# Optimization experiments

Measured on AMD Instinct MI355X. Metric: run time of the kernel, lower is better.

The kernel has to match this reference:

```python
import jax, jax.numpy as jnp
import numpy as np

B, LQ, LKV, D, H = 4, 1024, 2048, 1024, 16
HD = D // H
EPS = 1e-5
NEG = -1e9


def _layernorm(x, w, b):
    mu = jnp.mean(x, axis=-1, keepdims=True)
    var = jnp.mean(jnp.square(x - mu), axis=-1, keepdims=True)
    return (x - mu) * jax.lax.rsqrt(var + EPS) * w + b


def setup_inputs() -> dict:
    key = jax.random.key(0)
    ks = jax.random.split(key, 10)
    q = jax.random.normal(ks[0], (B, LQ, D), dtype=jnp.float32)
    kv = jax.random.normal(ks[1], (B, LKV, D), dtype=jnp.float32)
    # ragged kv lengths; mask True == padding
    lengths = jax.random.randint(ks[2], (B,), LKV // 4, LKV + 1)
    mask = jnp.arange(LKV)[None, :] >= lengths[:, None]  # [B, LKV] bool
    s = 1.0 / np.sqrt(D)
    params = dict(
        norm_q_w=jnp.ones((D,), jnp.float32),
        norm_q_b=jnp.zeros((D,), jnp.float32),
        norm_kv_w=jnp.ones((D,), jnp.float32),
        norm_kv_b=jnp.zeros((D,), jnp.float32),
        Wq=jax.random.normal(ks[3], (D, D), jnp.float32) * s,
        bq=jnp.zeros((D,), jnp.float32),
        Wkv=jax.random.normal(ks[4], (2 * D, D), jnp.float32) * s,
        bkv=jnp.zeros((2 * D,), jnp.float32),
        Wo=jax.random.normal(ks[5], (D, D), jnp.float32) * s,
        bo=jnp.zeros((D,), jnp.float32),
    )
    return dict(q=q, kv=kv, mask=mask, **params)


def reference(q, kv, mask, norm_q_w, norm_q_b, norm_kv_w, norm_kv_b, Wq, bq, Wkv, bkv, Wo, bo):
    q_res = q
    qn = _layernorm(q, norm_q_w, norm_q_b)
    kvn = _layernorm(kv, norm_kv_w, norm_kv_b)
    # projections
    qh = (qn @ Wq.T + bq).reshape(B, LQ, H, HD)
    kvp = (kvn @ Wkv.T + bkv).reshape(B, LKV, 2, H, HD)
    k, v = kvp[:, :, 0], kvp[:, :, 1]  # [B, LKV, H, HD]
    # masked cross attention (math-equivalent to varlen flash attn over unpadded kv)
    scale = 1.0 / np.sqrt(HD)
    scores = jnp.einsum('bqhd,bkhd->bhqk', qh, k) * scale
    scores = jnp.where(mask[:, None, None, :], NEG, scores)
    attn = jax.nn.softmax(scores, axis=-1)
    out = jnp.einsum('bhqk,bkhd->bqhd', attn, v).reshape(B, LQ, D)
    # out proj + residual (dropout is identity in eval)
    return q_res + (out @ Wo.T + bo)


if __name__ == '__main__':
    inp = setup_inputs()
    y = reference(**inp)
    print(y.shape, y.dtype)
```

## Files before the change

kernel.cpp:

```cpp
#include <hip/hip_runtime.h>

#define DEV __device__ __forceinline__

typedef unsigned short u16;
typedef float  floatx4 __attribute__((ext_vector_type(4)));
typedef unsigned int uintx2 __attribute__((ext_vector_type(2)));
typedef unsigned int uintx4 __attribute__((ext_vector_type(4)));
typedef __bf16 bf16x8 __attribute__((ext_vector_type(8)));

constexpr int cB = 4, cLQ = 1024, cLKV = 2048, cD = 1024, cH = 16, cHD = 64;

DEV u16 f2bf(float f) {
  unsigned u = __builtin_bit_cast(unsigned, f);
  u += 0x7fffu + ((u >> 16) & 1u);
  return (u16)(u >> 16);
}

DEV bf16x8 ld_frag(const u16* p) {
  uintx4 u = *(const uintx4*)p;
  return __builtin_bit_cast(bf16x8, u);
}

DEV floatx4 mfma16(bf16x8 a, bf16x8 b, floatx4 c) {
  return __builtin_amdgcn_mfma_f32_16x16x32_bf16(a, b, c, 0, 0, 0);
}

DEV float ex2(float x) { return __builtin_amdgcn_exp2f(x); }

DEV unsigned pkbf(float a, float b) {
  return (__builtin_bit_cast(unsigned, b) & 0xffff0000u) |
         (__builtin_bit_cast(unsigned, a) >> 16);
}

DEV void pl32(unsigned &a, unsigned &b) {
#if __has_builtin(__builtin_amdgcn_permlane32_swap)
  uintx2 r = __builtin_amdgcn_permlane32_swap(a, b, false, false);
  a = r[0]; b = r[1];
#else
  asm("v_permlane32_swap_b32 %0, %1" : "+v"(a), "+v"(b));
#endif
}
DEV void pl16(unsigned &a, unsigned &b) {
#if __has_builtin(__builtin_amdgcn_permlane16_swap)
  uintx2 r = __builtin_amdgcn_permlane16_swap(a, b, false, false);
  a = r[0]; b = r[1];
#else
  asm("v_permlane16_swap_b32 %0, %1" : "+v"(a), "+v"(b));
#endif
}

__global__ __launch_bounds__(256) void prep_kernel(
    const float* __restrict__ q, const float* __restrict__ kv,
    const float* __restrict__ nqw, const float* __restrict__ nqb,
    const float* __restrict__ nkw, const float* __restrict__ nkb,
    u16* __restrict__ qn, u16* __restrict__ kvn,
    const float* __restrict__ Wq, const float* __restrict__ Wkv,
    const float* __restrict__ Wo, u16* __restrict__ wqb,
    u16* __restrict__ wkvb, u16* __restrict__ wob,
    const void* __restrict__ mask, int* __restrict__ lens) {
  int bid = blockIdx.x, tid = threadIdx.x;
  if (bid < 3072) {
    int row = bid * 4 + (tid >> 6);
    int lane = tid & 63;
    const float* x; const float* w; const float* b; u16* dst;
    if (row < cB * cLQ) {
      x = q + (size_t)row * cD; w = nqw; b = nqb; dst = qn + (size_t)row * cD;
    } else {
      int r2 = row - cB * cLQ;
      x = kv + (size_t)r2 * cD; w = nkw; b = nkb; dst = kvn + (size_t)r2 * cD;
    }
    const float4* xf = (const float4*)x;
    float4 v[4];
    #pragma unroll
    for (int c = 0; c < 4; c++) v[c] = xf[lane + 64 * c];
    float s = 0.f;
    #pragma unroll
    for (int c = 0; c < 4; c++) s += (v[c].x + v[c].y) + (v[c].z + v[c].w);
    #pragma unroll
    for (int m = 1; m < 64; m <<= 1) s += __shfl_xor(s, m, 64);
    float mean = s * (1.f / cD);
    float ss = 0.f;
    #pragma unroll
    for (int c = 0; c < 4; c++) {
      v[c].x -= mean; v[c].y -= mean; v[c].z -= mean; v[c].w -= mean;
      ss += (v[c].x * v[c].x + v[c].y * v[c].y) +
            (v[c].z * v[c].z + v[c].w * v[c].w);
    }
    #pragma unroll
    for (int m = 1; m < 64; m <<= 1) ss += __shfl_xor(ss, m, 64);
    float rs = rsqrtf(ss * (1.f / cD) + 1e-5f);
    const float4* wf = (const float4*)w;
    const float4* bf = (const float4*)b;
    #pragma unroll
    for (int c = 0; c < 4; c++) {
      float4 wv = wf[lane + 64 * c];
      float4 bv = bf[lane + 64 * c];
      ushort4 o;
      o.x = f2bf(v[c].x * rs * wv.x + bv.x);
      o.y = f2bf(v[c].y * rs * wv.y + bv.y);
      o.z = f2bf(v[c].z * rs * wv.z + bv.z);
      o.w = f2bf(v[c].w * rs * wv.w + bv.w);
      ((ushort4*)dst)[lane + 64 * c] = o;
    }
  } else if (bid < 4096) {
    int base = (bid - 3072) * 1024;
    #pragma unroll
    for (int c = 0; c < 4; c++) {
      int gi = base + c * 256 + tid;
      const float* src; u16* dst; int off;
      if (gi < 262144)      { src = Wq;  dst = wqb;  off = gi; }
      else if (gi < 786432) { src = Wkv; dst = wkvb; off = gi - 262144; }
      else                  { src = Wo;  dst = wob;  off = gi - 786432; }
      float4 v = ((const float4*)src)[off];
      ushort4 o;
      o.x = f2bf(v.x); o.y = f2bf(v.y); o.z = f2bf(v.z); o.w = f2bf(v.w);
      ((ushort4*)dst)[off] = o;
    }
  } else {
    __shared__ int smode;
    __shared__ int cnt[cB];
    if (tid == 0) smode = 0;
    if (tid < cB) cnt[tid] = 0;
    __syncthreads();
    const unsigned* mi = (const unsigned*)mask;
    int bad = 0;
    for (int i = tid; i < cB * cLKV / 4; i += 256)
      if (mi[i] > 1u) bad = 1;
    if (bad) smode = 1;
    __syncthreads();
    if (smode == 0) {
      for (int b = 0; b < cB; b++) {
        int c = 0;
        for (int i = tid; i < cLKV; i += 256) c += (mi[(size_t)b * cLKV + i] == 0u);
        atomicAdd(&cnt[b], c);
      }
    } else {
      const unsigned char* m8 = (const unsigned char*)mask;
      for (int b = 0; b < cB; b++) {
        int c = 0;
        for (int i = tid; i < cLKV; i += 256) c += (m8[(size_t)b * cLKV + i] == 0);
        atomicAdd(&cnt[b], c);
      }
    }
    __syncthreads();
    if (tid < cB) lens[tid] = cnt[tid];
    if (tid == 0) {
      int ord[4] = {0, 1, 2, 3};
      #pragma unroll
      for (int a = 0; a < 3; a++)
        #pragma unroll
        for (int d = 0; d < 3; d++)
          if (cnt[ord[d]] < cnt[ord[d + 1]]) {
            int tswap = ord[d]; ord[d] = ord[d + 1]; ord[d + 1] = tswap;
          }
      #pragma unroll
      for (int a = 0; a < 4; a++) lens[4 + a] = ord[a];
    }
  }
}

struct TileCtx {
  int m16, quad, wr, wc;
};

DEV void gemm_mainloop(const u16* __restrict__ A, const u16* __restrict__ Bm,
                       int row0, int col0, int K, u16* As, u16* Bs,
                       const TileCtx& t, floatx4 (&acc)[4][4]) {
  int tid = threadIdx.x;
  int wave = tid >> 6, lane = tid & 63;
  int srow = wave * 16 + (lane >> 2);
  int sseg = (lane & 3) * 8;
  const u16* ga = A + (size_t)(row0 + srow) * K + sseg;
  const u16* gb = Bm + (size_t)(col0 + srow) * K + sseg;
  const size_t rstep = (size_t)64 * K;
  int woff = srow * 32 + sseg;

  uintx4 a0 = *(const uintx4*)ga;
  uintx4 a1 = *(const uintx4*)(ga + rstep);
  uintx4 b0 = *(const uintx4*)gb;
  uintx4 b1 = *(const uintx4*)(gb + rstep);
  *(uintx4*)(As + woff) = a0;
  *(uintx4*)(As + woff + 2048) = a1;
  *(uintx4*)(Bs + woff) = b0;
  *(uintx4*)(Bs + woff + 2048) = b1;
  a0 = *(const uintx4*)(ga + 32);
  a1 = *(const uintx4*)(ga + rstep + 32);
  b0 = *(const uintx4*)(gb + 32);
  b1 = *(const uintx4*)(gb + rstep + 32);
  __syncthreads();

  for (int k0 = 0; k0 < K; k0 += 32) {
    int cur = (k0 >> 5) & 1;
    const u16* rA = As + cur * 4096;
    const u16* rB = Bs + cur * 4096;
    bf16x8 af[4], bfr[4];
    #pragma unroll
    for (int i = 0; i < 4; i++)
      af[i] = ld_frag(&rA[(t.wr * 64 + i * 16 + t.m16) * 32 + t.quad * 8]);
    #pragma unroll
    for (int j = 0; j < 4; j++)
      bfr[j] = ld_frag(&rB[(t.wc * 64 + j * 16 + t.m16) * 32 + t.quad * 8]);
    if (k0 + 32 < K) {
      u16* nA = As + (cur ^ 1) * 4096 + woff;
      u16* nB = Bs + (cur ^ 1) * 4096 + woff;
      *(uintx4*)nA = a0;
      *(uintx4*)(nA + 2048) = a1;
      *(uintx4*)nB = b0;
      *(uintx4*)(nB + 2048) = b1;
      if (k0 + 64 < K) {
        a0 = *(const uintx4*)(ga + k0 + 64);
        a1 = *(const uintx4*)(ga + rstep + k0 + 64);
        b0 = *(const uintx4*)(gb + k0 + 64);
        b1 = *(const uintx4*)(gb + rstep + k0 + 64);
      }
    }
    #pragma unroll
    for (int i = 0; i < 4; i++)
      #pragma unroll
      for (int j = 0; j < 4; j++)
        acc[i][j] = mfma16(af[i], bfr[j], acc[i][j]);
    __syncthreads();
  }
}

__global__ __launch_bounds__(256) void proj_fused(
    const u16* __restrict__ qn, const u16* __restrict__ wqb,
    const float* __restrict__ bq, u16* __restrict__ qhb,
    const u16* __restrict__ kvn, const u16* __restrict__ wkvb,
    const float* __restrict__ bkv, u16* __restrict__ khb,
    u16* __restrict__ vthb, const int* __restrict__ lens) {
  __shared__ __align__(16) u16 As[2 * 128 * 32];
  __shared__ __align__(16) u16 Bs[2 * 128 * 32];
  int bid = blockIdx.x;
  int lane = threadIdx.x & 63;
  TileCtx t;
  t.m16 = lane & 15; t.quad = lane >> 4;
  int wave = threadIdx.x >> 6;
  t.wr = wave >> 1; t.wc = wave & 1;

  bool isQ = bid < 256;
  int row0, col0;
  const u16* A; const u16* Bm; const float* bias;
  if (isQ) {
    row0 = (bid >> 3) * 128; col0 = (bid & 7) * 128;
    A = qn; Bm = wqb; bias = bq;
  } else {
    int b2 = bid - 256;
    row0 = (b2 >> 4) * 128; col0 = (b2 & 15) * 128;
    A = kvn; Bm = wkvb; bias = bkv;
    if ((row0 & (cLKV - 1)) >= lens[row0 >> 11]) return;
  }

  floatx4 z = {0.f, 0.f, 0.f, 0.f};
  floatx4 acc[4][4];
  #pragma unroll
  for (int i = 0; i < 4; i++)
    #pragma unroll
    for (int j = 0; j < 4; j++) acc[i][j] = z;

  gemm_mainloop(A, Bm, row0, col0, cD, As, Bs, t, acc);

  #pragma unroll
  for (int j = 0; j < 4; j++) {
    int col = col0 + t.wc * 64 + j * 16 + t.m16;
    float bs = bias[col];
    if (isQ) {
      #pragma unroll
      for (int i = 0; i < 4; i++) {
        int crow = row0 + t.wr * 64 + i * 16 + t.quad * 4;
        #pragma unroll
        for (int r = 0; r < 4; r++)
          qhb[(size_t)(crow + r) * cD + col] =
              f2bf((acc[i][j][r] + bs) * 0.18033688f);
      }
    } else {
      bool isK = col < cD;
      int c2 = isK ? col : col - cD;
      int hh = c2 >> 6, dd = c2 & 63;
      #pragma unroll
      for (int i = 0; i < 4; i++) {
        int crow = row0 + t.wr * 64 + i * 16 + t.quad * 4;
        int bb = crow >> 11, kvp = crow & (cLKV - 1);
        if (isK) {
          u16* dst = khb + ((size_t)(bb * cH + hh) * cLKV + kvp) * 64 + dd;
          #pragma unroll
          for (int r = 0; r < 4; r++) dst[(size_t)r * 64] = f2bf(acc[i][j][r] + bs);
        } else {
          u16* dst = vthb + ((size_t)(bb * cH + hh) * 64 + dd) * cLKV + kvp;
          ushort4 o;
          o.x = f2bf(acc[i][j][0] + bs);
          o.y = f2bf(acc[i][j][1] + bs);
          o.z = f2bf(acc[i][j][2] + bs);
          o.w = f2bf(acc[i][j][3] + bs);
          *(ushort4*)dst = o;
        }
      }
    }
  }
}

__global__ __launch_bounds__(256) void gemm_o(
    const u16* __restrict__ A, const u16* __restrict__ Bm,
    const float* __restrict__ bias, const float* __restrict__ res,
    float* __restrict__ Cout, int N, int K) {
  __shared__ __align__(16) u16 As[2 * 64 * 32];
  __shared__ __align__(16) u16 Bs[2 * 128 * 32];
  int lane = threadIdx.x & 63;
  int m16 = lane & 15, quad = lane >> 4;
  int wave = threadIdx.x >> 6;
  int wr = wave >> 1, wc = wave & 1;
  int row0 = blockIdx.y * 64, col0 = blockIdx.x * 128;

  int tid = threadIdx.x;
  int srow = tid >> 2;
  int sseg = (tid & 3) * 8;
  const u16* ga = A + (size_t)(row0 + srow) * K + sseg;
  const u16* gb = Bm + (size_t)(col0 + srow) * K + sseg;
  const size_t rstep = (size_t)64 * K;
  int woff = srow * 32 + sseg;

  uintx4 a0 = *(const uintx4*)ga;
  uintx4 b0 = *(const uintx4*)gb;
  uintx4 b1 = *(const uintx4*)(gb + rstep);
  *(uintx4*)(As + woff) = a0;
  *(uintx4*)(Bs + woff) = b0;
  *(uintx4*)(Bs + woff + 2048) = b1;
  a0 = *(const uintx4*)(ga + 32);
  b0 = *(const uintx4*)(gb + 32);
  b1 = *(const uintx4*)(gb + rstep + 32);
  __syncthreads();

  floatx4 z = {0.f, 0.f, 0.f, 0.f};
  floatx4 acc[2][4];
  #pragma unroll
  for (int i = 0; i < 2; i++)
    #pragma unroll
    for (int j = 0; j < 4; j++) acc[i][j] = z;

  for (int k0 = 0; k0 < K; k0 += 32) {
    int cur = (k0 >> 5) & 1;
    const u16* rA = As + cur * 2048;
    const u16* rB = Bs + cur * 4096;
    bf16x8 af[2], bfr[4];
    #pragma unroll
    for (int i = 0; i < 2; i++)
      af[i] = ld_frag(&rA[(wr * 32 + i * 16 + m16) * 32 + quad * 8]);
    #pragma unroll
    for (int j = 0; j < 4; j++)
      bfr[j] = ld_frag(&rB[(wc * 64 + j * 16 + m16) * 32 + quad * 8]);
    if (k0 + 32 < K) {
      u16* nA = As + (cur ^ 1) * 2048 + woff;
      u16* nB = Bs + (cur ^ 1) * 4096 + woff;
      *(uintx4*)nA = a0;
      *(uintx4*)nB = b0;
      *(uintx4*)(nB + 2048) = b1;
      if (k0 + 64 < K) {
        a0 = *(const uintx4*)(ga + k0 + 64);
        b0 = *(const uintx4*)(gb + k0 + 64);
        b1 = *(const uintx4*)(gb + rstep + k0 + 64);
      }
    }
    #pragma unroll
    for (int i = 0; i < 2; i++)
      #pragma unroll
      for (int j = 0; j < 4; j++)
        acc[i][j] = mfma16(af[i], bfr[j], acc[i][j]);
    __syncthreads();
  }

  #pragma unroll
  for (int j = 0; j < 4; j++) {
    int col = col0 + wc * 64 + j * 16 + m16;
    float bs = bias[col];
    #pragma unroll
    for (int i = 0; i < 2; i++) {
      int crow = row0 + wr * 32 + i * 16 + quad * 4;
      #pragma unroll
      for (int r = 0; r < 4; r++) {
        size_t idx = (size_t)(crow + r) * N + col;
        Cout[idx] = acc[i][j][r] + bs + res[idx];
      }
    }
  }
}

constexpr int KS = 72;

template<bool MASK>
DEV void attn_compute(int k0, int len, const u16* __restrict__ Kt,
                      const u16* __restrict__ Vt,
                      const bf16x8 (&qf)[2][2], int m16, int quad,
                      float (&lsum)[2], floatx4 (&accO)[2][4]) {
  floatx4 z = {0.f, 0.f, 0.f, 0.f};
  bf16x8 kf[4][2];
  #pragma unroll
  for (int t = 0; t < 4; t++) {
    kf[t][0] = ld_frag(&Kt[(t * 16 + m16) * KS + quad * 8]);
    kf[t][1] = ld_frag(&Kt[(t * 16 + m16) * KS + 32 + quad * 8]);
  }
  floatx4 s[2][4];
  #pragma unroll
  for (int g = 0; g < 2; g++)
    #pragma unroll
    for (int t = 0; t < 4; t++) {
      floatx4 tt = z;
      tt = mfma16(kf[t][0], qf[g][0], tt);
      tt = mfma16(kf[t][1], qf[g][1], tt);
      s[g][t] = tt;
    }
  bf16x8 ap0[2], ap1[2];
  #pragma unroll
  for (int g = 0; g < 2; g++) {
    unsigned p[4][2];
    #pragma unroll
    for (int t = 0; t < 4; t++) {
      float e0, e1, e2, e3;
      if (MASK) {
        int key = k0 + t * 16 + quad * 4;
        e0 = (key     < len) ? ex2(s[g][t][0]) : 0.f;
        e1 = (key + 1 < len) ? ex2(s[g][t][1]) : 0.f;
        e2 = (key + 2 < len) ? ex2(s[g][t][2]) : 0.f;
        e3 = (key + 3 < len) ? ex2(s[g][t][3]) : 0.f;
      } else {
        e0 = ex2(s[g][t][0]);
        e1 = ex2(s[g][t][1]);
        e2 = ex2(s[g][t][2]);
        e3 = ex2(s[g][t][3]);
      }
      lsum[g] += (e0 + e1) + (e2 + e3);
      p[t][0] = pkbf(e0, e1);
      p[t][1] = pkbf(e2, e3);
    }
    unsigned a0 = p[0][0], b0 = p[1][0]; pl32(a0, b0); pl16(a0, b0);
    unsigned a1 = p[0][1], b1 = p[1][1]; pl32(a1, b1); pl16(a1, b1);
    uintx4 lo = {a0, a1, b0, b1};
    unsigned c0 = p[2][0], d0 = p[3][0]; pl32(c0, d0); pl16(c0, d0);
    unsigned c1 = p[2][1], d1 = p[3][1]; pl32(c1, d1); pl16(c1, d1);
    uintx4 hi = {c0, c1, d0, d1};
    ap0[g] = __builtin_bit_cast(bf16x8, lo);
    ap1[g] = __builtin_bit_cast(bf16x8, hi);
  }
  #pragma unroll
  for (int db = 0; db < 4; db++) {
    bf16x8 bv0 = ld_frag(&Vt[(db * 16 + m16) * KS + quad * 8]);
    bf16x8 bv1 = ld_frag(&Vt[(db * 16 + m16) * KS + 32 + quad * 8]);
    #pragma unroll
    for (int g = 0; g < 2; g++) {
      accO[g][db] = mfma16(ap0[g], bv0, accO[g][db]);
      accO[g][db] = mfma16(ap1[g], bv1, accO[g][db]);
    }
  }
}

__global__ __launch_bounds__(256) void attn_kernel(
    const u16* __restrict__ qh, const u16* __restrict__ kh,
    const u16* __restrict__ vth, const int* __restrict__ lens,
    u16* __restrict__ out) {
  int bid = blockIdx.x;
  int r = bid >> 7;
  int rank = r ^ (r >> 1);
  int b = lens[4 + rank];
  int combo = bid & 127;
  int h = combo >> 3;
  int qt = combo & 7;
  int len = lens[b];
  int wave = threadIdx.x >> 6, lane = threadIdx.x & 63;
  int m16 = lane & 15, quad = lane >> 4;

  __shared__ __align__(16) u16 Kt[64 * KS];
  __shared__ __align__(16) u16 Vt[64 * KS];

  int q0 = qt * 128 + wave * 32;
  const u16* qp = qh + ((size_t)(b * cLQ + q0 + m16) * cH + h) * cHD;
  bf16x8 qf[2][2];
  qf[0][0] = ld_frag(qp + quad * 8);
  qf[0][1] = ld_frag(qp + 32 + quad * 8);
  qf[1][0] = ld_frag(qp + (size_t)16 * cD + quad * 8);
  qf[1][1] = ld_frag(qp + (size_t)16 * cD + 32 + quad * 8);

  const u16* kbase = kh + (size_t)(b * cH + h) * cLKV * cHD;
  const u16* vbase = vth + (size_t)(b * cH + h) * cHD * cLKV;

  int srow = threadIdx.x >> 3;
  int sseg = threadIdx.x & 7;
  const u16* kg = kbase + (size_t)srow * cHD + sseg * 8;
  const u16* vg = vbase + (size_t)srow * cLKV + sseg * 8;

  float lsum[2] = {0.f, 0.f};
  floatx4 z = {0.f, 0.f, 0.f, 0.f};
  floatx4 accO[2][4] = {{z, z, z, z}, {z, z, z, z}};

  int nch = (len + 63) >> 6;
  uintx4 ka  = *(const uintx4*)kg;
  uintx4 kb2 = *(const uintx4*)(kg + (size_t)32 * cHD);
  uintx4 va  = *(const uintx4*)vg;
  uintx4 vb  = *(const uintx4*)(vg + (size_t)32 * cLKV);

  for (int c = 0; c < nch; c++) {
    int k0 = c * 64;
    __syncthreads();
    *(uintx4*)&Kt[srow * KS + sseg * 8] = ka;
    *(uintx4*)&Kt[(srow + 32) * KS + sseg * 8] = kb2;
    *(uintx4*)&Vt[srow * KS + sseg * 8] = va;
    *(uintx4*)&Vt[(srow + 32) * KS + sseg * 8] = vb;
    if (c + 1 < nch) {
      int kn = k0 + 64;
      ka  = *(const uintx4*)(kg + (size_t)kn * cHD);
      kb2 = *(const uintx4*)(kg + (size_t)(kn + 32) * cHD);
      va  = *(const uintx4*)(vg + kn);
      vb  = *(const uintx4*)(vg + (size_t)32 * cLKV + kn);
    }
    __syncthreads();
    if (k0 + 64 <= len)
      attn_compute<false>(k0, len, Kt, Vt, qf, m16, quad, lsum, accO);
    else
      attn_compute<true>(k0, len, Kt, Vt, qf, m16, quad, lsum, accO);
  }

  #pragma unroll
  for (int g = 0; g < 2; g++) {
    float tsum = lsum[g];
    tsum += __shfl_xor(tsum, 16, 64);
    tsum += __shfl_xor(tsum, 32, 64);
    #pragma unroll
    for (int rr = 0; rr < 4; rr++) {
      float inv = 1.0f / __shfl(tsum, quad * 4 + rr, 16);
      int qg = q0 + g * 16 + quad * 4 + rr;
      size_t base = ((size_t)(b * cLQ + qg) * cH + h) * cHD;
      #pragma unroll
      for (int db = 0; db < 4; db++)
        out[base + db * 16 + m16] = f2bf(accO[g][db][rr] * inv);
    }
  }
}

extern "C" void kernel_launch(void* const* d_in, const int* in_sizes, int n_in,
                              void* d_out, int out_size, void* d_ws, size_t ws_size,
                              hipStream_t stream) {
  const float* q    = (const float*)d_in[0];
  const float* kv   = (const float*)d_in[1];
  const void*  mask = d_in[2];
  const float* nqw  = (const float*)d_in[3];
  const float* nqb  = (const float*)d_in[4];
  const float* nkw  = (const float*)d_in[5];
  const float* nkb  = (const float*)d_in[6];
  const float* Wq   = (const float*)d_in[7];
  const float* bq   = (const float*)d_in[8];
  const float* Wkv  = (const float*)d_in[9];
  const float* bkv  = (const float*)d_in[10];
  const float* Wo   = (const float*)d_in[11];
  const float* bo   = (const float*)d_in[12];
  float* out = (float*)d_out;

  char* w = (char*)d_ws;
  int* lens = (int*)w;       w += 256;
  u16* qn   = (u16*)w;       w += (size_t)cB * cLQ * cD * 2;
  u16* kvn  = (u16*)w;       w += (size_t)cB * cLKV * cD * 2;
  u16* wqb  = (u16*)w;       w += (size_t)cD * cD * 2;
  u16* wkvb = (u16*)w;       w += (size_t)2 * cD * cD * 2;
  u16* wob  = (u16*)w;       w += (size_t)cD * cD * 2;
  u16* qhb  = (u16*)w;       w += (size_t)cB * cLQ * cD * 2;
  u16* khb  = (u16*)w;       w += (size_t)cB * cH * cLKV * cHD * 2;
  u16* vthb = (u16*)w;       w += (size_t)cB * cH * cHD * cLKV * 2;
  u16* aob  = (u16*)w;

  prep_kernel<<<4097, 256, 0, stream>>>(
      q, kv, nqw, nqb, nkw, nkb, qn, kvn,
      Wq, Wkv, Wo, wqb, wkvb, wob, mask, lens);
  proj_fused<<<1280, 256, 0, stream>>>(
      qn, wqb, bq, qhb, kvn, wkvb, bkv, khb, vthb, lens);
  attn_kernel<<<512, 256, 0, stream>>>(
      qhb, khb, vthb, lens, aob);
  gemm_o<<<dim3(cD / 128, cB * cLQ / 64), 256, 0, stream>>>(
      aob, wob, bo, q, out, cD, cD);
}
```

Measured before the change: 262.5 us.

## Use direct global-to-LDS loads with triple-buffered pipeline in projection GEMM

Replaces the register-staged double-buffered mainloop of the Q/KV projection GEMM with global_load_lds direct-to-LDS copies and a three-slot ring buffer. Loads are issued two K-steps ahead and each step ends with a waitcnt+barrier. This removes the VGPR round trip and the LDS store instructions, and leaves more loads in flight. In exchange it uses more shared memory (three slots instead of two) and relies on hand-written vmcnt accounting being correct.

Measured after the change: 256.8 us. 1.02x faster.

```diff
diff --git a/kernel.cpp b/kernel.cpp
--- a/kernel.cpp
+++ b/kernel.cpp
@@ -48,6 +48,15 @@
   asm("v_permlane16_swap_b32 %0, %1" : "+v"(a), "+v"(b));
 #endif
 }
+
+DEV void gload16(const u16* g, u16* l) {
+  __builtin_amdgcn_global_load_lds(
+      (const __attribute__((address_space(1))) void*)g,
+      (__attribute__((address_space(3))) void*)l, 16, 0, 0);
+}
+
+#define WB4() asm volatile("s_waitcnt vmcnt(4)\n\ts_barrier" ::: "memory")
+#define WB0() asm volatile("s_waitcnt vmcnt(0)\n\ts_barrier" ::: "memory")
 
 __global__ __launch_bounds__(256) void prep_kernel(
     const float* __restrict__ q, const float* __restrict__ kv,
@@ -159,84 +168,20 @@
   }
 }
 
-struct TileCtx {
-  int m16, quad, wr, wc;
-};
-
-DEV void gemm_mainloop(const u16* __restrict__ A, const u16* __restrict__ Bm,
-                       int row0, int col0, int K, u16* As, u16* Bs,
-                       const TileCtx& t, floatx4 (&acc)[4][4]) {
-  int tid = threadIdx.x;
-  int wave = tid >> 6, lane = tid & 63;
-  int srow = wave * 16 + (lane >> 2);
-  int sseg = (lane & 3) * 8;
-  const u16* ga = A + (size_t)(row0 + srow) * K + sseg;
-  const u16* gb = Bm + (size_t)(col0 + srow) * K + sseg;
-  const size_t rstep = (size_t)64 * K;
-  int woff = srow * 32 + sseg;
-
-  uintx4 a0 = *(const uintx4*)ga;
-  uintx4 a1 = *(const uintx4*)(ga + rstep);
-  uintx4 b0 = *(const uintx4*)gb;
-  uintx4 b1 = *(const uintx4*)(gb + rstep);
-  *(uintx4*)(As + woff) = a0;
-  *(uintx4*)(As + woff + 2048) = a1;
-  *(uintx4*)(Bs + woff) = b0;
-  *(uintx4*)(Bs + woff + 2048) = b1;
-  a0 = *(const uintx4*)(ga + 32);
-  a1 = *(const uintx4*)(ga + rstep + 32);
-  b0 = *(const uintx4*)(gb + 32);
-  b1 = *(const uintx4*)(gb + rstep + 32);
-  __syncthreads();
-
-  for (int k0 = 0; k0 < K; k0 += 32) {
-    int cur = (k0 >> 5) & 1;
-    const u16* rA = As + cur * 4096;
-    const u16* rB = Bs + cur * 4096;
-    bf16x8 af[4], bfr[4];
-    #pragma unroll
-    for (int i = 0; i < 4; i++)
-      af[i] = ld_frag(&rA[(t.wr * 64 + i * 16 + t.m16) * 32 + t.quad * 8]);
-    #pragma unroll
-    for (int j = 0; j < 4; j++)
-      bfr[j] = ld_frag(&rB[(t.wc * 64 + j * 16 + t.m16) * 32 + t.quad * 8]);
-    if (k0 + 32 < K) {
-      u16* nA = As + (cur ^ 1) * 4096 + woff;
-      u16* nB = Bs + (cur ^ 1) * 4096 + woff;
-      *(uintx4*)nA = a0;
-      *(uintx4*)(nA + 2048) = a1;
-      *(uintx4*)nB = b0;
-      *(uintx4*)(nB + 2048) = b1;
-      if (k0 + 64 < K) {
-        a0 = *(const uintx4*)(ga + k0 + 64);
-        a1 = *(const uintx4*)(ga + rstep + k0 + 64);
-        b0 = *(const uintx4*)(gb + k0 + 64);
-        b1 = *(const uintx4*)(gb + rstep + k0 + 64);
-      }
-    }
-    #pragma unroll
-    for (int i = 0; i < 4; i++)
-      #pragma unroll
-      for (int j = 0; j < 4; j++)
-        acc[i][j] = mfma16(af[i], bfr[j], acc[i][j]);
-    __syncthreads();
-  }
-}
-
 __global__ __launch_bounds__(256) void proj_fused(
     const u16* __restrict__ qn, const u16* __restrict__ wqb,
     const float* __restrict__ bq, u16* __restrict__ qhb,
     const u16* __restrict__ kvn, const u16* __restrict__ wkvb,
     const float* __restrict__ bkv, u16* __restrict__ khb,
     u16* __restrict__ vthb, const int* __restrict__ lens) {
-  __shared__ __align__(16) u16 As[2 * 128 * 32];
-  __shared__ __align__(16) u16 Bs[2 * 128 * 32];
+  __shared__ __align__(16) u16 As[3 * 128 * 32];
+  __shared__ __align__(16) u16 Bs[3 * 128 * 32];
   int bid = blockIdx.x;
-  int lane = threadIdx.x & 63;
-  TileCtx t;
-  t.m16 = lane & 15; t.quad = lane >> 4;
-  int wave = threadIdx.x >> 6;
-  t.wr = wave >> 1; t.wc = wave & 1;
+  int tid = threadIdx.x;
+  int lane = tid & 63;
+  int m16 = lane & 15, quad = lane >> 4;
+  int wave = tid >> 6;
+  int wr = wave >> 1, wc = wave & 1;
 
   bool isQ = bid < 256;
   int row0, col0;
@@ -250,6 +195,30 @@
     A = kvn; Bm = wkvb; bias = bkv;
     if ((row0 & (cLKV - 1)) >= lens[row0 >> 11]) return;
   }
+  const int K = cD;
+  constexpr int T = cD / 32;
+
+  int l4 = lane >> 2;
+  int l2 = (lane & 3) * 8;
+  const u16* ga0 = A + (size_t)(row0 + wave * 16 + l4) * K + l2;
+  const u16* ga1 = ga0 + (size_t)64 * K;
+  const u16* gb0 = Bm + (size_t)(col0 + wave * 16 + l4) * K + l2;
+  const u16* gb1 = gb0 + (size_t)64 * K;
+  u16* dAw = As + wave * 512;
+  u16* dBw = Bs + wave * 512;
+
+#define ISSUE(kk, slot) do { \
+    u16* dA_ = dAw + (slot) * 4096; \
+    u16* dB_ = dBw + (slot) * 4096; \
+    gload16(ga0 + (kk), dA_); \
+    gload16(ga1 + (kk), dA_ + 2048); \
+    gload16(gb0 + (kk), dB_); \
+    gload16(gb1 + (kk), dB_ + 2048); \
+  } while (0)
+
+  ISSUE(0, 0);
+  ISSUE(32, 1);
+  WB4();
 
   floatx4 z = {0.f, 0.f, 0.f, 0.f};
   floatx4 acc[4][4];
@@ -258,16 +227,37 @@
     #pragma unroll
     for (int j = 0; j < 4; j++) acc[i][j] = z;
 
-  gemm_mainloop(A, Bm, row0, col0, cD, As, Bs, t, acc);
+  #pragma unroll 3
+  for (int i = 0; i < T; i++) {
+    int slot = i % 3;
+    if (i + 2 < T) ISSUE((i + 2) * 32, (i + 2) % 3);
+    const u16* rA = As + slot * 4096;
+    const u16* rB = Bs + slot * 4096;
+    bf16x8 af[4], bfr[4];
+    #pragma unroll
+    for (int ii = 0; ii < 4; ii++)
+      af[ii] = ld_frag(&rA[(wr * 64 + ii * 16 + m16) * 32 + quad * 8]);
+    #pragma unroll
+    for (int j = 0; j < 4; j++)
+      bfr[j] = ld_frag(&rB[(wc * 64 + j * 16 + m16) * 32 + quad * 8]);
+    #pragma unroll
+    for (int ii = 0; ii < 4; ii++)
+      #pragma unroll
+      for (int j = 0; j < 4; j++)
+        acc[ii][j] = mfma16(af[ii], bfr[j], acc[ii][j]);
+    if (i + 2 < T) WB4();
+    else if (i + 1 < T) WB0();
+  }
+#undef ISSUE
 
   #pragma unroll
   for (int j = 0; j < 4; j++) {
-    int col = col0 + t.wc * 64 + j * 16 + t.m16;
+    int col = col0 + wc * 64 + j * 16 + m16;
     float bs = bias[col];
     if (isQ) {
       #pragma unroll
       for (int i = 0; i < 4; i++) {
-        int crow = row0 + t.wr * 64 + i * 16 + t.quad * 4;
+        int crow = row0 + wr * 64 + i * 16 + quad * 4;
         #pragma unroll
         for (int r = 0; r < 4; r++)
           qhb[(size_t)(crow + r) * cD + col] =
@@ -279,7 +269,7 @@
       int hh = c2 >> 6, dd = c2 & 63;
       #pragma unroll
       for (int i = 0; i < 4; i++) {
-        int crow = row0 + t.wr * 64 + i * 16 + t.quad * 4;
+        int crow = row0 + wr * 64 + i * 16 + quad * 4;
         int bb = crow >> 11, kvp = crow & (cLKV - 1);
         if (isK) {
           u16* dst = khb + ((size_t)(bb * cH + hh) * cLKV + kvp) * 64 + dd;
```
